# Performance work log

Measured on AMD Instinct MI355X. Metric: run time of the kernel, lower is better.

## Reference

```python
import jax, jax.numpy as jnp
import numpy as np

# Surrogate-gradient spike (ActFun_adp from DH-SNN): Heaviside fwd, multi-Gaussian bwd
GAMMA, LENS, SCALE, HIGHT = 0.5, 0.5, 6.0, 0.15
VTH = 1.0

def _gauss(x, mu, sigma):
    return jnp.exp(-((x - mu) ** 2) / (2.0 * sigma ** 2)) / (jnp.sqrt(2.0 * jnp.pi) * sigma)

@jax.custom_vjp
def spike_fn(x):
    return (x > 0).astype(x.dtype)

def _spike_fwd(x):
    return spike_fn(x), x

def _spike_bwd(x, g):
    temp = (_gauss(x, 0.0, LENS) * (1.0 + HIGHT)
            - _gauss(x, LENS, SCALE * LENS) * HIGHT
            - _gauss(x, -LENS, SCALE * LENS) * HIGHT)
    return (g * temp * GAMMA,)

spike_fn.defvjp(_spike_fwd, _spike_bwd)

B, T, IN, H, OUT = 128, 1000, 700, 512, 20

def setup_inputs() -> dict:
    key = jax.random.key(0)
    ks = jax.random.split(key, 10)
    lim1 = float(1.0 / np.sqrt(IN))
    lim2 = float(1.0 / np.sqrt(H))
    return {
        "x": jax.random.uniform(ks[0], (B, T, IN), jnp.float32),
        "W1": jax.random.uniform(ks[1], (H, IN), jnp.float32, -lim1, lim1),
        "b1": jax.random.uniform(ks[2], (H,), jnp.float32, -lim1, lim1),
        "tau_m1": jax.random.uniform(ks[3], (H,), jnp.float32, 0.0, 4.0),
        "tau_n1": jax.random.uniform(ks[4], (H,), jnp.float32, 0.0, 4.0),
        "W2": jax.random.uniform(ks[5], (OUT, H), jnp.float32, -lim2, lim2),
        "b2": jax.random.uniform(ks[6], (OUT,), jnp.float32, -lim2, lim2),
        "tau_m2": jax.random.uniform(ks[7], (OUT,), jnp.float32, 0.0, 4.0),
        "mem1_0": jax.random.uniform(ks[8], (B, H), jnp.float32),   # set_neuron_state uses rand init
        "mem2_0": jax.random.uniform(ks[9], (B, OUT), jnp.float32),
    }

def reference(x, W1, b1, tau_m1, tau_n1, W2, b2, tau_m2, mem1_0, mem2_0):
    alpha1 = jax.nn.sigmoid(tau_m1)   # [H] membrane decay
    beta1 = jax.nn.sigmoid(tau_n1)    # [H] dendritic decay (branch=1 -> branch dim collapsed)
    alpha2 = jax.nn.sigmoid(tau_m2)   # [OUT] readout decay
    # Input projection is time-invariant: one big GEMM instead of T small ones.
    proj = jnp.einsum('bti,hi->bth', x, W1) + b1  # [B,T,H]

    def step(carry, p_t):
        mem1, spike1, d_in, mem2 = carry
        d_in = beta1 * d_in + (1.0 - beta1) * p_t                       # dendritic filter
        mem1 = mem1 * alpha1 + (1.0 - alpha1) * d_in - VTH * spike1      # LIF soft reset
        spike1 = spike_fn(mem1 - VTH)
        mem2 = mem2 * alpha2 + (1.0 - alpha2) * (spike1 @ W2.T + b2)     # leaky readout
        return (mem1, spike1, d_in, mem2), mem2

    init = (mem1_0, jnp.zeros_like(mem1_0), jnp.zeros_like(mem1_0), mem2_0)
    _, outs = jax.lax.scan(step, init, jnp.swapaxes(proj, 0, 1))  # scan over time
    return jnp.swapaxes(outs, 0, 1)  # [B, T, OUT]
```

## Files before the change

### kernel.cpp

```cpp
#include <hip/hip_runtime.h>
#include <stdint.h>

#define Bd   128
#define Td   1000
#define INd  700
#define Hd   512
#define OUTd 20
#define Md   (Bd * Td)
#define KPAD 704
#define KIT  22
#define KH   1408

typedef _Float16 f16;
typedef f16 f16x4 __attribute__((ext_vector_type(4)));
typedef f16 f16x8 __attribute__((ext_vector_type(8)));
typedef float f32x4 __attribute__((ext_vector_type(4)));

__device__ __forceinline__ void gld_lds16(const void* g, void* l) {
  __builtin_amdgcn_global_load_lds(
      (__attribute__((address_space(1))) void*)(g),
      (__attribute__((address_space(3))) void*)(l), 16, 0, 0);
}

__global__ __launch_bounds__(256) void pack_kernel(
    const float* __restrict__ src, f16* __restrict__ dst, int nrows) {
  const int t = blockIdx.x * 256 + threadIdx.x;
  if (t >= nrows * 88) return;
  const int m = t / 88;
  const int rem = t - m * 88;
  const int kt = rem >> 2;
  const int lc = rem & 3;
  const int k0 = kt * 32 + lc * 8;
  const float* sp = src + (size_t)m * INd + k0;
  float v[8];
  if (k0 + 8 <= INd) {
    const float4 v0 = *(const float4*)sp;
    const float4 v1 = *(const float4*)(sp + 4);
    v[0] = v0.x; v[1] = v0.y; v[2] = v0.z; v[3] = v0.w;
    v[4] = v1.x; v[5] = v1.y; v[6] = v1.z; v[7] = v1.w;
  } else {
#pragma unroll
    for (int u = 0; u < 8; ++u) v[u] = (k0 + u < INd) ? sp[u] : 0.f;
  }
  f16x8 h1, h2;
#pragma unroll
  for (int u = 0; u < 8; ++u) {
    const f16 a = (f16)v[u];
    h1[u] = a;
    h2[u] = (f16)(v[u] - (float)a);
  }
  const int s = m & 7;
  f16* out = dst + (size_t)m * KH + (size_t)kt * 64;
  *(f16x8*)(out + ((lc ^ s) << 3)) = h1;
  *(f16x8*)(out + (((lc + 4) ^ s) << 3)) = h2;
}

#define SBAR __builtin_amdgcn_sched_barrier(0)

#define LOAD_FRAGS(S, MH, NH, AB, BB)                                   \
  _Pragma("unroll")                                                     \
  for (int mi = 0; mi < 4; ++mi) {                                      \
    const int rb = (wm0 + (MH) * 64 + mi * 16 + fr) << 6;               \
    a1##S[mi] = *(const f16x8*)&(AB)[rb + o1];                          \
    a2##S[mi] = *(const f16x8*)&(AB)[rb + o2];                          \
  }                                                                     \
  _Pragma("unroll")                                                     \
  for (int nj = 0; nj < 2; ++nj) {                                      \
    const int cb = (wn0 + (NH) * 32 + nj * 16 + fr) << 6;               \
    b1##S[nj] = *(const f16x8*)&(BB)[cb + o1];                          \
    b2##S[nj] = *(const f16x8*)&(BB)[cb + o2];                          \
  }

#define MFMA_PHASE(S, MH, NH)                                           \
  __builtin_amdgcn_s_setprio(1);                                        \
  _Pragma("unroll")                                                     \
  for (int mi = 0; mi < 4; ++mi)                                        \
  _Pragma("unroll")                                                     \
  for (int nj = 0; nj < 2; ++nj) {                                      \
    f32x4 a = acc[(MH) * 4 + mi][(NH) * 2 + nj];                        \
    a = __builtin_amdgcn_mfma_f32_16x16x32_f16(a1##S[mi], b1##S[nj], a, 0, 0, 0); \
    a = __builtin_amdgcn_mfma_f32_16x16x32_f16(a1##S[mi], b2##S[nj], a, 0, 0, 0); \
    a = __builtin_amdgcn_mfma_f32_16x16x32_f16(a2##S[mi], b1##S[nj], a, 0, 0, 0); \
    acc[(MH) * 4 + mi][(NH) * 2 + nj] = a;                              \
  }                                                                     \
  __builtin_amdgcn_s_setprio(0);

#define STAGE_A(NB, GO)                                                 \
  _Pragma("unroll")                                                     \
  for (int j = 0; j < 4; ++j)                                           \
    gld_lds16(Ag + (size_t)j * (64 * KH) + (GO), &As[NB][tid * 8 + j * 4096]);

#define STAGE_B(NB, GO)                                                 \
  _Pragma("unroll")                                                     \
  for (int j = 0; j < 4; ++j)                                           \
    gld_lds16(Bg + (size_t)j * (64 * KH) + (GO), &Bs[NB][tid * 8 + j * 4096]);

__global__ __launch_bounds__(512, 2) void gemm1_kernel(
    const f16* __restrict__ Xp, const f16* __restrict__ Wp,
    const float* __restrict__ b1, float* __restrict__ proj) {
  __shared__ __align__(16) f16 As[2][256 * 64];
  __shared__ __align__(16) f16 Bs[2][256 * 64];
  const int tid = threadIdx.x;

  const int l = blockIdx.x;
  const int bb = (l & 7) * 125 + (l >> 3);
  const int m0 = (bb >> 1) << 8;
  const int n0 = (bb & 1) << 8;

  const int srow = tid >> 3, sc = tid & 7;
  const f16* Ag = Xp + (size_t)(m0 + srow) * KH + (sc << 3);
  const f16* Bg = Wp + (size_t)(n0 + srow) * KH + (sc << 3);

  const int wv = tid >> 6, lane = tid & 63;
  const int wm0 = (wv >> 2) << 7;
  const int wn0 = (wv & 3) << 6;
  const int fr = lane & 15;
  const int fq = lane >> 4;
  const int swz = (fr & 7) << 4;
  const int o1 = ((fq << 4) ^ swz) >> 1;
  const int o2 = (((fq + 4) << 4) ^ swz) >> 1;

  f32x4 acc[8][4];
#pragma unroll
  for (int i = 0; i < 8; ++i)
#pragma unroll
    for (int j = 0; j < 4; ++j) acc[i][j] = (f32x4){0.f, 0.f, 0.f, 0.f};

  f16x8 a1E[4], a2E[4], b1E[2], b2E[2];
  f16x8 a1O[4], a2O[4], b1O[2], b2O[2];

  STAGE_A(0, 0);
  STAGE_B(0, 0);
  asm volatile("s_waitcnt vmcnt(0)" ::: "memory");
  __builtin_amdgcn_sched_barrier(0);
  __builtin_amdgcn_s_barrier();
  LOAD_FRAGS(E, 0, 0, As[0], Bs[0]);

#pragma unroll 1
  for (int t = 0; t < KIT; ++t) {
    const f16* Ac = As[t & 1];
    const f16* Bc = Bs[t & 1];
    const int nb = (t & 1) ^ 1;
    const bool pf = (t + 1 < KIT);
    const size_t go = (size_t)(t + 1) << 6;

    LOAD_FRAGS(O, 0, 1, Ac, Bc);
    if (pf) { STAGE_A(nb, go); }
    SBAR;
    MFMA_PHASE(E, 0, 0);
    SBAR;
    LOAD_FRAGS(E, 1, 0, Ac, Bc);
    if (pf) { STAGE_B(nb, go); }
    SBAR;
    MFMA_PHASE(O, 0, 1);
    SBAR;
    LOAD_FRAGS(O, 1, 1, Ac, Bc);
    SBAR;
    MFMA_PHASE(E, 1, 0);
    SBAR;
    if (pf) {
      asm volatile("s_waitcnt vmcnt(0) lgkmcnt(0)" ::: "memory");
      __builtin_amdgcn_sched_barrier(0);
      __builtin_amdgcn_s_barrier();
      LOAD_FRAGS(E, 0, 0, As[nb], Bs[nb]);
    }
    SBAR;
    MFMA_PHASE(O, 1, 1);
    SBAR;
  }

#pragma unroll
  for (int ni = 0; ni < 4; ++ni) {
    const int n = n0 + wn0 + ni * 16 + fr;
    const float bias = b1[n];
#pragma unroll
    for (int mi = 0; mi < 8; ++mi) {
      const int mb = m0 + wm0 + mi * 16 + (fq << 2);
      float* p = proj + (size_t)mb * Hd + n;
#pragma unroll
      for (int rr = 0; rr < 4; ++rr)
        p[(size_t)rr * Hd] = acc[mi][ni][rr] + bias;
    }
  }
}

__global__ __launch_bounds__(256) void w1split_kernel(
    const float* __restrict__ W1, f16* __restrict__ W1a,
    f16* __restrict__ W1b) {
  const int idx = blockIdx.x * 256 + threadIdx.x;
  if (idx >= 512 * KPAD) return;
  const int n = idx / KPAD, k = idx - n * KPAD;
  const float v = (k < INd) ? W1[n * INd + k] : 0.f;
  const f16 h1 = (f16)v;
  const f16 h2 = (f16)(v - (float)h1);
  W1a[idx] = h1;
  W1b[idx] = h2;
}

__global__ __launch_bounds__(256) void gemm1_fb_kernel(
    const float* __restrict__ X, const f16* __restrict__ W1a,
    const f16* __restrict__ W1b, const float* __restrict__ b1,
    float* __restrict__ proj) {
  __shared__ __align__(16) f16 A1s[128 * 40];
  __shared__ __align__(16) f16 A2s[128 * 40];
  __shared__ __align__(16) f16 B1s[128 * 40];
  __shared__ __align__(16) f16 B2s[128 * 40];

  const int tid = threadIdx.x;
  const int n0 = blockIdx.x * 128;
  const int m0 = blockIdx.y * 128;

  const int srow = tid >> 1;
  const int skq  = (tid & 1) << 4;

  const float* Xp  = X + (size_t)(m0 + srow) * INd;
  const f16*   Bap = W1a + (size_t)(n0 + srow) * KPAD + skq;
  const f16*   Bbp = W1b + (size_t)(n0 + srow) * KPAD + skq;

  const int wv = tid >> 6, lane = tid & 63;
  const int wm0 = (wv >> 1) * 64, wn0 = (wv & 1) * 64;
  const int fr = lane & 15;
  const int fq = lane >> 4;

  f32x4 acc[4][4];
#pragma unroll
  for (int i = 0; i < 4; ++i)
#pragma unroll
    for (int j = 0; j < 4; ++j) acc[i][j] = (f32x4){0.f, 0.f, 0.f, 0.f};

  const float4 z4 = make_float4(0.f, 0.f, 0.f, 0.f);
  float4 ax[4];
  f16x8 bq1[2], bq2[2];

#pragma unroll
  for (int i = 0; i < 4; ++i) ax[i] = *(const float4*)(Xp + skq + 4 * i);
  bq1[0] = *(const f16x8*)(Bap);     bq1[1] = *(const f16x8*)(Bap + 8);
  bq2[0] = *(const f16x8*)(Bbp);     bq2[1] = *(const f16x8*)(Bbp + 8);

#pragma unroll 1
  for (int it = 0; it < KIT; ++it) {
    __syncthreads();
#pragma unroll
    for (int i = 0; i < 4; ++i) {
      const float4 v = ax[i];
      f16x4 h1, h2;
      h1.x = (f16)v.x; h2.x = (f16)(v.x - (float)h1.x);
      h1.y = (f16)v.y; h2.y = (f16)(v.y - (float)h1.y);
      h1.z = (f16)v.z; h2.z = (f16)(v.z - (float)h1.z);
      h1.w = (f16)v.w; h2.w = (f16)(v.w - (float)h1.w);
      *(f16x4*)&A1s[srow * 40 + skq + 4 * i] = h1;
      *(f16x4*)&A2s[srow * 40 + skq + 4 * i] = h2;
    }
    *(f16x8*)&B1s[srow * 40 + skq]     = bq1[0];
    *(f16x8*)&B1s[srow * 40 + skq + 8] = bq1[1];
    *(f16x8*)&B2s[srow * 40 + skq]     = bq2[0];
    *(f16x8*)&B2s[srow * 40 + skq + 8] = bq2[1];
    __syncthreads();
    if (it + 1 < KIT) {
      const int k0 = (it + 1) * 32;
#pragma unroll
      for (int i = 0; i < 4; ++i) {
        const int k = k0 + skq + 4 * i;
        ax[i] = (k + 4 <= INd) ? *(const float4*)(Xp + k) : z4;
      }
      bq1[0] = *(const f16x8*)(Bap + k0);
      bq1[1] = *(const f16x8*)(Bap + k0 + 8);
      bq2[0] = *(const f16x8*)(Bbp + k0);
      bq2[1] = *(const f16x8*)(Bbp + k0 + 8);
    }
    f16x8 a1f[4], a2f[4], b1f[4], b2f[4];
#pragma unroll
    for (int mi = 0; mi < 4; ++mi) {
      const int off = (wm0 + mi * 16 + fr) * 40 + fq * 8;
      a1f[mi] = *(const f16x8*)&A1s[off];
      a2f[mi] = *(const f16x8*)&A2s[off];
    }
#pragma unroll
    for (int ni = 0; ni < 4; ++ni) {
      const int off = (wn0 + ni * 16 + fr) * 40 + fq * 8;
      b1f[ni] = *(const f16x8*)&B1s[off];
      b2f[ni] = *(const f16x8*)&B2s[off];
    }
#pragma unroll
    for (int mi = 0; mi < 4; ++mi)
#pragma unroll
      for (int ni = 0; ni < 4; ++ni) {
        acc[mi][ni] = __builtin_amdgcn_mfma_f32_16x16x32_f16(
            a1f[mi], b1f[ni], acc[mi][ni], 0, 0, 0);
        acc[mi][ni] = __builtin_amdgcn_mfma_f32_16x16x32_f16(
            a1f[mi], b2f[ni], acc[mi][ni], 0, 0, 0);
        acc[mi][ni] = __builtin_amdgcn_mfma_f32_16x16x32_f16(
            a2f[mi], b1f[ni], acc[mi][ni], 0, 0, 0);
      }
  }

#pragma unroll
  for (int ni = 0; ni < 4; ++ni) {
    const int n = n0 + wn0 + ni * 16 + fr;
    const float bias = b1[n];
#pragma unroll
    for (int mi = 0; mi < 4; ++mi) {
      const int mb = m0 + wm0 + mi * 16 + fq * 4;
      float* p = proj + (size_t)mb * Hd + n;
#pragma unroll
      for (int r = 0; r < 4; ++r)
        p[(size_t)r * Hd] = acc[mi][ni][r] + bias;
    }
  }
}

#define S1_PHASE(QC, QN, T0)                                      \
  {                                                               \
    const int tp_ = (T0) + 24;                                    \
    _Pragma("unroll")                                             \
    for (int u = 0; u < 8; ++u) {                                 \
      const int tt = (tp_ + u < Td) ? (tp_ + u) : (Td - 1);       \
      buf[QN][u] = pp[(size_t)tt * Hd];                           \
    }                                                             \
    _Pragma("unroll")                                             \
    for (int u = 0; u < 8; ++u) {                                 \
      const float pv = buf[QC][u];                                \
      d = bn * d + ombn * pv;                                     \
      mem = am * mem + omam * d - s;                              \
      const bool fire = mem > 1.0f;                               \
      s = fire ? 1.f : 0.f;                                       \
      const unsigned long long msk = __ballot(fire);              \
      if (lane == 0) sp[(size_t)((T0) + u) * 8] = msk;            \
    }                                                             \
  }

__global__ __launch_bounds__(256) void scan1_kernel(
    const float* __restrict__ proj, const float* __restrict__ tau_m1,
    const float* __restrict__ tau_n1, const float* __restrict__ mem1_0,
    unsigned long long* __restrict__ spk) {
  const int gid = blockIdx.x * 256 + threadIdx.x;
  const int b = gid >> 9;
  const int h = gid & 511;
  const float am = 1.f / (1.f + expf(-tau_m1[h]));
  const float bn = 1.f / (1.f + expf(-tau_n1[h]));
  const float omam = 1.f - am, ombn = 1.f - bn;
  float mem = mem1_0[(b << 9) | h];
  float d = 0.f, s = 0.f;
  const float* pp = proj + (size_t)b * Td * Hd + h;
  unsigned long long* sp = spk + (size_t)b * Td * 8 + (h >> 6);
  const int lane = threadIdx.x & 63;

  float buf[4][8];
#pragma unroll
  for (int q = 0; q < 3; ++q)
#pragma unroll
    for (int u = 0; u < 8; ++u)
      buf[q][u] = pp[(size_t)(q * 8 + u) * Hd];

#pragma unroll 1
  for (int t0 = 0; t0 < 992; t0 += 32) {
    S1_PHASE(0, 3, t0);
    S1_PHASE(1, 0, t0 + 8);
    S1_PHASE(2, 1, t0 + 16);
    S1_PHASE(3, 2, t0 + 24);
  }
  S1_PHASE(0, 3, 992);
}

__global__ __launch_bounds__(256) void gemm2_kernel(
    const unsigned long long* __restrict__ spk, const float* __restrict__ W2,
    const float* __restrict__ b2, float* __restrict__ R, int Mtotal) {
  __shared__ float W2s[Hd * OUTd];
  const int tid = threadIdx.x;
  for (int idx = tid; idx < Hd * OUTd; idx += 256) {
    const int h = idx / OUTd, o = idx - h * OUTd;
    W2s[idx] = W2[o * Hd + h];
  }
  __syncthreads();
  const int wave = tid >> 6, lane = tid & 63;
  const int mg = lane / OUTd;
  const int o = lane - mg * OUTd;
  if (mg >= 3) return;
  const float bias = b2[o];
  const int mbase = blockIdx.x * 96 + wave * 24 + mg;
#pragma unroll 1
  for (int i = 0; i < 8; ++i) {
    const int m = mbase + i * 3;
    if (m >= Mtotal) break;
    float r = bias;
    const unsigned long long* mp = spk + (size_t)m * 8;
#pragma unroll
    for (int c = 0; c < 8; ++c) {
      unsigned long long mask = mp[c];
      const float* wrow = W2s + (c << 6) * OUTd + o;
      while (mask) {
        const int j = __builtin_ctzll(mask);
        mask &= mask - 1;
        r += wrow[j * OUTd];
      }
    }
    R[(size_t)m * OUTd + o] = r;
  }
}

__global__ __launch_bounds__(256) void scan2_kernel(
    const float* __restrict__ R, const float* __restrict__ tau_m2,
    const float* __restrict__ mem2_0, float* __restrict__ out) {
  __shared__ float leS[8][20];
  __shared__ float stS[8][20];
  const int b = blockIdx.x;
  const int tid = threadIdx.x;
  const int c = tid / OUTd;
  const int o = tid - c * OUTd;
  const bool active = tid < 160;
  float a2 = 0.f, oma2 = 0.f;
  if (active) {
    a2 = 1.f / (1.f + expf(-tau_m2[o]));
    oma2 = 1.f - a2;
  }
  const float* Rb = R + (size_t)b * Td * OUTd;
  float* Ob = out + (size_t)b * Td * OUTd;
  const int t0 = c * 125;

  if (active) {
    float m = 0.f;
    for (int u = 0; u < 125; ++u)
      m = a2 * m + oma2 * Rb[(size_t)(t0 + u) * OUTd + o];
    leS[c][o] = m;
  }
  __syncthreads();
  if (tid < OUTd) {
    const float a = 1.f / (1.f + expf(-tau_m2[tid]));
    float aL = 1.f;
    for (int i = 0; i < 125; ++i) aL *= a;
    float m = mem2_0[b * OUTd + tid];
    for (int cc = 0; cc < 8; ++cc) {
      stS[cc][tid] = m;
      m = aL * m + leS[cc][tid];
    }
  }
  __syncthreads();
  if (active) {
    float m = stS[c][o];
    for (int u = 0; u < 125; ++u) {
      m = a2 * m + oma2 * Rb[(size_t)(t0 + u) * OUTd + o];
      Ob[(size_t)(t0 + u) * OUTd + o] = m;
    }
  }
}

extern "C" void kernel_launch(void* const* d_in, const int* in_sizes, int n_in,
                              void* d_out, int out_size, void* d_ws, size_t ws_size,
                              hipStream_t stream) {
  const float* x      = (const float*)d_in[0];
  const float* W1     = (const float*)d_in[1];
  const float* b1     = (const float*)d_in[2];
  const float* tau_m1 = (const float*)d_in[3];
  const float* tau_n1 = (const float*)d_in[4];
  const float* W2     = (const float*)d_in[5];
  const float* b2     = (const float*)d_in[6];
  const float* tau_m2 = (const float*)d_in[7];
  const float* mem1_0 = (const float*)d_in[8];
  const float* mem2_0 = (const float*)d_in[9];
  float* out = (float*)d_out;

  const size_t proj_b = (size_t)Md * Hd * sizeof(float);
  const size_t xp_b   = (size_t)Md * KH * sizeof(f16);
  const size_t wp_b   = (size_t)512 * KH * sizeof(f16);
  const size_t spk_b  = (size_t)Md * 8 * sizeof(unsigned long long);

  float* proj = (float*)d_ws;

  if (ws_size >= proj_b + xp_b + wp_b) {
    f16* Xpk = (f16*)((char*)d_ws + proj_b);
    f16* Wpk = (f16*)((char*)d_ws + proj_b + xp_b);
    unsigned long long* spk = (unsigned long long*)((char*)d_ws + proj_b);
    float* R = (float*)((char*)d_ws + proj_b + spk_b);

    pack_kernel<<<dim3(Md * 88 / 256), 256, 0, stream>>>(x, Xpk, Md);
    pack_kernel<<<dim3(512 * 88 / 256), 256, 0, stream>>>(W1, Wpk, 512);
    gemm1_kernel<<<dim3((Hd / 256) * (Md / 256)), 512, 0, stream>>>(Xpk, Wpk,
                                                                    b1, proj);
    scan1_kernel<<<dim3(Bd * Hd / 256), 256, 0, stream>>>(proj, tau_m1, tau_n1,
                                                          mem1_0, spk);
    gemm2_kernel<<<dim3((Md + 95) / 96), 256, 0, stream>>>(spk, W2, b2, R, Md);
    scan2_kernel<<<dim3(Bd), 256, 0, stream>>>(R, tau_m2, mem2_0, out);
  } else {
    unsigned long long* spk =
        (unsigned long long*)((char*)d_ws + proj_b);
    float* R = (float*)((char*)spk + spk_b);
    f16* W1a = (f16*)R;
    f16* W1b = W1a + 512 * KPAD;

    w1split_kernel<<<dim3((512 * KPAD + 255) / 256), 256, 0, stream>>>(W1, W1a,
                                                                       W1b);
    gemm1_fb_kernel<<<dim3(Hd / 128, Md / 128), 256, 0, stream>>>(x, W1a, W1b,
                                                                  b1, proj);
    scan1_kernel<<<dim3(Bd * Hd / 256), 256, 0, stream>>>(proj, tau_m1, tau_n1,
                                                          mem1_0, spk);
    gemm2_kernel<<<dim3((Md + 95) / 96), 256, 0, stream>>>(spk, W2, b2, R, Md);
    scan2_kernel<<<dim3(Bd), 256, 0, stream>>>(R, tau_m2, mem2_0, out);
  }
}
```

Before: 926.6 us.

## Switch GEMM1 to 32x32x16 MFMA tiles and deepen LDS prefetch pipeline

Replaces the 16x16x32 MFMA fragment scheme with 32x32x16 MFMAs, so each wave issues fewer, larger matrix instructions and loads fewer LDS fragments per K-tile. It also restructures the pipeline: A and B staging are merged and issued two K-tiles ahead right after the barrier, instead of being split across phases one tile ahead. The epilogue mapping is rewritten for the 32x32 accumulator layout. The risk is that the new swizzle offsets and the store pattern may hurt LDS bank conflicts or write coalescing.

After: 977.1 us. 1.05x slower.

```diff
diff --git a/kernel.cpp b/kernel.cpp
--- a/kernel.cpp
+++ b/kernel.cpp
@@ -15,6 +15,7 @@
 typedef f16 f16x4 __attribute__((ext_vector_type(4)));
 typedef f16 f16x8 __attribute__((ext_vector_type(8)));
 typedef float f32x4 __attribute__((ext_vector_type(4)));
+typedef float f32x16 __attribute__((ext_vector_type(16)));
 
 __device__ __forceinline__ void gld_lds16(const void* g, void* l) {
   __builtin_amdgcn_global_load_lds(
@@ -57,43 +58,40 @@
 
 #define SBAR __builtin_amdgcn_sched_barrier(0)
 
-#define LOAD_FRAGS(S, MH, NH, AB, BB)                                   \
+#define LOAD_FR(S, O1, O2, AB, BB)                                      \
   _Pragma("unroll")                                                     \
-  for (int mi = 0; mi < 4; ++mi) {                                      \
-    const int rb = (wm0 + (MH) * 64 + mi * 16 + fr) << 6;               \
-    a1##S[mi] = *(const f16x8*)&(AB)[rb + o1];                          \
-    a2##S[mi] = *(const f16x8*)&(AB)[rb + o2];                          \
+  for (int mt = 0; mt < 4; ++mt) {                                      \
+    const int rb = (wm0 + mt * 32 + l31) << 6;                          \
+    a1##S[mt] = *(const f16x8*)&(AB)[rb + (O1)];                        \
+    a2##S[mt] = *(const f16x8*)&(AB)[rb + (O2)];                        \
   }                                                                     \
   _Pragma("unroll")                                                     \
-  for (int nj = 0; nj < 2; ++nj) {                                      \
-    const int cb = (wn0 + (NH) * 32 + nj * 16 + fr) << 6;               \
-    b1##S[nj] = *(const f16x8*)&(BB)[cb + o1];                          \
-    b2##S[nj] = *(const f16x8*)&(BB)[cb + o2];                          \
-  }
-
-#define MFMA_PHASE(S, MH, NH)                                           \
+  for (int nt = 0; nt < 2; ++nt) {                                      \
+    const int cb = (wn0 + nt * 32 + l31) << 6;                          \
+    b1##S[nt] = *(const f16x8*)&(BB)[cb + (O1)];                        \
+    b2##S[nt] = *(const f16x8*)&(BB)[cb + (O2)];                        \
+  }
+
+#define MM(S)                                                           \
   __builtin_amdgcn_s_setprio(1);                                        \
   _Pragma("unroll")                                                     \
-  for (int mi = 0; mi < 4; ++mi)                                        \
+  for (int mt = 0; mt < 4; ++mt)                                        \
   _Pragma("unroll")                                                     \
-  for (int nj = 0; nj < 2; ++nj) {                                      \
-    f32x4 a = acc[(MH) * 4 + mi][(NH) * 2 + nj];                        \
-    a = __builtin_amdgcn_mfma_f32_16x16x32_f16(a1##S[mi], b1##S[nj], a, 0, 0, 0); \
-    a = __builtin_amdgcn_mfma_f32_16x16x32_f16(a1##S[mi], b2##S[nj], a, 0, 0, 0); \
-    a = __builtin_amdgcn_mfma_f32_16x16x32_f16(a2##S[mi], b1##S[nj], a, 0, 0, 0); \
-    acc[(MH) * 4 + mi][(NH) * 2 + nj] = a;                              \
+  for (int nt = 0; nt < 2; ++nt) {                                      \
+    f32x16 a = acc[mt][nt];                                             \
+    a = __builtin_amdgcn_mfma_f32_32x32x16_f16(a1##S[mt], b1##S[nt], a, 0, 0, 0); \
+    a = __builtin_amdgcn_mfma_f32_32x32x16_f16(a1##S[mt], b2##S[nt], a, 0, 0, 0); \
+    a = __builtin_amdgcn_mfma_f32_32x32x16_f16(a2##S[mt], b1##S[nt], a, 0, 0, 0); \
+    acc[mt][nt] = a;                                                    \
   }                                                                     \
   __builtin_amdgcn_s_setprio(0);
 
-#define STAGE_A(NB, GO)                                                 \
+#define STAGE_AB(NB, GO)                                                \
   _Pragma("unroll")                                                     \
-  for (int j = 0; j < 4; ++j)                                           \
-    gld_lds16(Ag + (size_t)j * (64 * KH) + (GO), &As[NB][tid * 8 + j * 4096]);
-
-#define STAGE_B(NB, GO)                                                 \
-  _Pragma("unroll")                                                     \
-  for (int j = 0; j < 4; ++j)                                           \
-    gld_lds16(Bg + (size_t)j * (64 * KH) + (GO), &Bs[NB][tid * 8 + j * 4096]);
+  for (int j = 0; j < 4; ++j) {                                         \
+    gld_lds16(Ag + (size_t)j * (64 * KH) + (GO), &As[NB][tid * 8 + j * 4096]); \
+    gld_lds16(Bg + (size_t)j * (64 * KH) + (GO), &Bs[NB][tid * 8 + j * 4096]); \
+  }
 
 __global__ __launch_bounds__(512, 2) void gemm1_kernel(
     const f16* __restrict__ Xp, const f16* __restrict__ Wp,
@@ -114,72 +112,68 @@
   const int wv = tid >> 6, lane = tid & 63;
   const int wm0 = (wv >> 2) << 7;
   const int wn0 = (wv & 3) << 6;
-  const int fr = lane & 15;
-  const int fq = lane >> 4;
-  const int swz = (fr & 7) << 4;
-  const int o1 = ((fq << 4) ^ swz) >> 1;
-  const int o2 = (((fq + 4) << 4) ^ swz) >> 1;
-
-  f32x4 acc[8][4];
-#pragma unroll
-  for (int i = 0; i < 8; ++i)
-#pragma unroll
-    for (int j = 0; j < 4; ++j) acc[i][j] = (f32x4){0.f, 0.f, 0.f, 0.f};
+  const int l31 = lane & 31;
+  const int hk  = lane >> 5;
+  const int sw  = lane & 7;
+  const int oE1 = (((0 + hk) ^ sw) << 3);
+  const int oE2 = (((4 + hk) ^ sw) << 3);
+  const int oO1 = (((2 + hk) ^ sw) << 3);
+  const int oO2 = (((6 + hk) ^ sw) << 3);
+
+  f32x16 acc[4][2];
+#pragma unroll
+  for (int i = 0; i < 4; ++i)
+#pragma unroll
+    for (int j = 0; j < 2; ++j) acc[i][j] = (f32x16)0.f;
 
   f16x8 a1E[4], a2E[4], b1E[2], b2E[2];
   f16x8 a1O[4], a2O[4], b1O[2], b2O[2];
 
-  STAGE_A(0, 0);
-  STAGE_B(0, 0);
+  STAGE_AB(0, 0);
   asm volatile("s_waitcnt vmcnt(0)" ::: "memory");
   __builtin_amdgcn_sched_barrier(0);
   __builtin_amdgcn_s_barrier();
-  LOAD_FRAGS(E, 0, 0, As[0], Bs[0]);
+  LOAD_FR(E, oE1, oE2, As[0], Bs[0]);
+  STAGE_AB(1, 64);
 
 #pragma unroll 1
   for (int t = 0; t < KIT; ++t) {
     const f16* Ac = As[t & 1];
     const f16* Bc = Bs[t & 1];
     const int nb = (t & 1) ^ 1;
-    const bool pf = (t + 1 < KIT);
-    const size_t go = (size_t)(t + 1) << 6;
-
-    LOAD_FRAGS(O, 0, 1, Ac, Bc);
-    if (pf) { STAGE_A(nb, go); }
+
+    LOAD_FR(O, oO1, oO2, Ac, Bc);
     SBAR;
-    MFMA_PHASE(E, 0, 0);
+    MM(E);
     SBAR;
-    LOAD_FRAGS(E, 1, 0, Ac, Bc);
-    if (pf) { STAGE_B(nb, go); }
-    SBAR;
-    MFMA_PHASE(O, 0, 1);
-    SBAR;
-    LOAD_FRAGS(O, 1, 1, Ac, Bc);
-    SBAR;
-    MFMA_PHASE(E, 1, 0);
-    SBAR;
-    if (pf) {
+
+    if (t + 1 < KIT) {
       asm volatile("s_waitcnt vmcnt(0) lgkmcnt(0)" ::: "memory");
       __builtin_amdgcn_sched_barrier(0);
       __builtin_amdgcn_s_barrier();
-      LOAD_FRAGS(E, 0, 0, As[nb], Bs[nb]);
+      if (t + 2 < KIT) {
+        const size_t go2 = (size_t)(t + 2) << 6;
+        STAGE_AB(t & 1, go2);
+      }
+      LOAD_FR(E, oE1, oE2, As[nb], Bs[nb]);
     }
     SBAR;
-    MFMA_PHASE(O, 1, 1);
+    MM(O);
     SBAR;
   }
 
 #pragma unroll
-  for (int ni = 0; ni < 4; ++ni) {
-    const int n = n0 + wn0 + ni * 16 + fr;
+  for (int nt = 0; nt < 2; ++nt) {
+    const int n = n0 + wn0 + nt * 32 + l31;
     const float bias = b1[n];
 #pragma unroll
-    for (int mi = 0; mi < 8; ++mi) {
-      const int mb = m0 + wm0 + mi * 16 + (fq << 2);
-      float* p = proj + (size_t)mb * Hd + n;
-#pragma unroll
-      for (int rr = 0; rr < 4; ++rr)
-        p[(size_t)rr * Hd] = acc[mi][ni][rr] + bias;
+    for (int mt = 0; mt < 4; ++mt) {
+      const int mb = m0 + wm0 + mt * 32 + 4 * hk;
+#pragma unroll
+      for (int r = 0; r < 16; ++r) {
+        const int m = mb + (r & 3) + 8 * (r >> 2);
+        proj[(size_t)m * Hd + n] = acc[mt][nt][r] + bias;
+      }
     }
   }
 }
```
